# Performance work log

Measured on AMD Instinct MI355X. Metric: run time of the kernel, lower is better.

The kernel has to match this reference:

```python
import jax, jax.numpy as jnp
import numpy as np

B, T, V = 4, 2048, 2048
D, H, L = 512, 8, 4
HD = D // H


def setup_inputs() -> dict:
    key = jax.random.key(0)
    ks = jax.random.split(key, 8)
    inp = {
        "x": jax.random.normal(ks[0], (B, T, V), dtype=jnp.float32),
        "token_embedding": jax.random.normal(ks[1], (D, V), dtype=jnp.float32),
        "position_embedding": jax.random.normal(ks[2], (T, D), dtype=jnp.float32),
        "Wk": jax.random.normal(ks[3], (L, D, D), dtype=jnp.float32),
        "Wq": jax.random.normal(ks[4], (L, D, D), dtype=jnp.float32),
        "Wv": jax.random.normal(ks[5], (L, D, D), dtype=jnp.float32),
        "Wp": jax.random.normal(ks[6], (L, D, D), dtype=jnp.float32),
        "readout": jax.random.normal(ks[7], (V, D), dtype=jnp.float32),
    }
    return inp


def _attention_block(h, wk, wq, wv, wp):
    # h: [B, T, D]; weights [D, D] (inner_dim == D since head_dim*num_heads == D)
    b, t, c = h.shape
    s = c ** (-0.5)

    def proj(w):
        # F.linear(h, w) = h @ w.T -> [B,T,D] -> [B,H,T,HD], scaled by C^{-1/2}
        return (jnp.einsum('btc,dc->btd', h, w) * s).reshape(b, t, H, HD).transpose(0, 2, 1, 3)

    q, k, v = proj(wq), proj(wk), proj(wv)
    scores = jnp.einsum('bhqd,bhkd->bhqk', q, k) * (HD ** (-0.5))  # [B,H,T,T]
    attn = jax.nn.softmax(scores, axis=-1)
    out = jnp.einsum('bhqk,bhkd->bhqd', attn, v)  # [B,H,T,HD]
    out = out.transpose(0, 2, 1, 3).reshape(b, t, c)
    # projection.size(-1) == inner_dim == D
    return jnp.einsum('btc,oc->bto', out, wp) * (c ** (-0.5))


def reference(x, token_embedding, position_embedding, Wk, Wq, Wv, Wp, readout):
    b, t, c = x.shape  # c == vocab_size
    tok = jnp.einsum('btv,dv->btd', x, token_embedding) * (c ** (-0.5))
    h = tok + position_embedding[:t]
    for l in range(L):
        h = _attention_block(h, Wk[l], Wq[l], Wv[l], Wp[l])
    # logits on last token; readout.size(-1) == D
    logits = jnp.einsum('bd,vd->bv', h[:, -1, :], readout) * (D ** (-0.5))
    return logits
```

## Files before the change

kernel.cpp:

```cpp
#include <hip/hip_runtime.h>
#include <math.h>

typedef __attribute__((ext_vector_type(4)))  float    f32x4;
typedef __attribute__((ext_vector_type(16))) float    f32x16;
typedef __attribute__((ext_vector_type(2)))  _Float16 f16x2;
typedef __attribute__((ext_vector_type(4)))  _Float16 f16x4;
typedef __attribute__((ext_vector_type(8)))  _Float16 f16x8;
typedef __attribute__((ext_vector_type(4)))  unsigned u32x4;

constexpr int Bc  = 4;
constexpr int Tc  = 2048;
constexpr int Vc  = 2048;
constexpr int Dc  = 512;
constexpr int Hc  = 8;
constexpr int HDc = 64;
constexpr int Lc  = 4;
constexpr size_t SZe = (size_t)Bc * Tc * Dc;

constexpr float SM_C = 12.0f;

__device__ __forceinline__ void gload_lds16(const _Float16* g, _Float16* s) {
    __builtin_amdgcn_global_load_lds(
        (const __attribute__((address_space(1))) void*)g,
        (__attribute__((address_space(3))) void*)s,
        16, 0, 0);
}

__device__ __forceinline__ unsigned cvt_pk_u(float a, float b) {
    return __builtin_bit_cast(unsigned, __builtin_amdgcn_cvt_pkrtz(a, b));
}

__global__ __launch_bounds__(256) void cvt_k(
    const float* __restrict__ in, _Float16* __restrict__ out, int n4)
{
    for (int i = blockIdx.x * 256 + threadIdx.x; i < n4; i += gridDim.x * 256) {
        float4 v = ((const float4*)in)[i];
        f16x4 h = {(_Float16)v.x, (_Float16)v.y, (_Float16)v.z, (_Float16)v.w};
        *(f16x4*)&out[(size_t)i * 4] = h;
    }
}

__global__ __launch_bounds__(256) void cvtW_k(
    const float* __restrict__ a, const float* __restrict__ b,
    const float* __restrict__ c, const float* __restrict__ d,
    _Float16* __restrict__ oa, _Float16* __restrict__ ob,
    _Float16* __restrict__ oc, _Float16* __restrict__ od, int n4)
{
    const float* in; _Float16* out;
    switch (blockIdx.y) {
        case 0:  in = a; out = oa; break;
        case 1:  in = b; out = ob; break;
        case 2:  in = c; out = oc; break;
        default: in = d; out = od; break;
    }
    for (int i = blockIdx.x * 256 + threadIdx.x; i < n4; i += gridDim.x * 256) {
        float4 v = ((const float4*)in)[i];
        f16x4 h = {(_Float16)v.x, (_Float16)v.y, (_Float16)v.z, (_Float16)v.w};
        *(f16x4*)&out[(size_t)i * 4] = h;
    }
}


template<bool QKV>
__global__ __launch_bounds__(256) void gemm_f16(
    const _Float16* __restrict__ A,
    const _Float16* __restrict__ W0, const _Float16* __restrict__ W1,
    const _Float16* __restrict__ W2,
    void* __restrict__ C0, const float* __restrict__ pos,
    int K, float scA, float scB)
{
    __shared__ __align__(16) _Float16 LA[2][128 * 64];
    __shared__ __align__(16) _Float16 LB[2][64 * 64];

    const int tid = threadIdx.x;
    const int w  = tid >> 6, l = tid & 63;
    const int li = l & 15,  lg = l >> 4;
    const int wm = w >> 1,  wn = w & 1;
    const int m0 = blockIdx.x * 128;

    int sec = 0, n0;
    const _Float16* Wb;
    if (QKV) {
        sec = blockIdx.y >> 3; n0 = (blockIdx.y & 7) * 64;
        Wb = (sec == 0) ? W0 : ((sec == 1) ? W1 : W2);
    } else {
        n0 = blockIdx.y * 64; Wb = W0;
    }
    const float scale = (sec == 0) ? scA : scB;

    const _Float16* srcA[4];
    const _Float16* srcB[2];
#pragma unroll
    for (int i = 0; i < 4; ++i) {
        const int d = i * 4096 + tid * 16;
        const int r = d >> 7, cb = (d & 127) ^ ((r & 7) << 4);
        srcA[i] = A + (size_t)(m0 + r) * K + (cb >> 1);
    }
#pragma unroll
    for (int i = 0; i < 2; ++i) {
        const int d = i * 4096 + tid * 16;
        const int r = d >> 7, cb = (d & 127) ^ ((r & 7) << 4);
        srcB[i] = Wb + (size_t)(n0 + r) * K + (cb >> 1);
    }

    auto stage = [&](int b) {
#pragma unroll
        for (int i = 0; i < 4; ++i) { gload_lds16(srcA[i], &LA[b][i * 2048 + tid * 8]); srcA[i] += 64; }
#pragma unroll
        for (int i = 0; i < 2; ++i) { gload_lds16(srcB[i], &LB[b][i * 2048 + tid * 8]); srcB[i] += 64; }
    };

    f32x4 acc[4][2];
#pragma unroll
    for (int i = 0; i < 4; ++i)
#pragma unroll
        for (int j = 0; j < 2; ++j) acc[i][j] = (f32x4){0.f, 0.f, 0.f, 0.f};

    auto compute = [&](int b) {
        const char* Ab = (const char*)&LA[b][0];
        const char* Bb = (const char*)&LB[b][0];
        f16x8 af[4][2], bf[2][2];
#pragma unroll
        for (int mb = 0; mb < 4; ++mb) {
            const int row = wm * 64 + mb * 16 + li, sz = (row & 7) << 4;
#pragma unroll
            for (int fi = 0; fi < 2; ++fi)
                af[mb][fi] = *(const f16x8*)(Ab + row * 128 + ((fi * 64 + lg * 16) ^ sz));
        }
#pragma unroll
        for (int nb = 0; nb < 2; ++nb) {
            const int row = wn * 32 + nb * 16 + li, sz = (row & 7) << 4;
#pragma unroll
            for (int fi = 0; fi < 2; ++fi)
                bf[nb][fi] = *(const f16x8*)(Bb + row * 128 + ((fi * 64 + lg * 16) ^ sz));
        }
#pragma unroll
        for (int mb = 0; mb < 4; ++mb)
#pragma unroll
            for (int nb = 0; nb < 2; ++nb)
#pragma unroll
                for (int fi = 0; fi < 2; ++fi)
                    acc[mb][nb] = __builtin_amdgcn_mfma_f32_16x16x32_f16(
                        af[mb][fi], bf[nb][fi], acc[mb][nb], 0, 0, 0);
    };

    const int NTk = K >> 6;
    stage(0);
    for (int kt = 0; kt < NTk; ++kt) {
        const int cur = kt & 1;
        if (kt + 1 < NTk) {
            stage(cur ^ 1);
            asm volatile("s_waitcnt vmcnt(6)" ::: "memory");
        } else {
            asm volatile("s_waitcnt vmcnt(0)" ::: "memory");
        }
        __builtin_amdgcn_s_barrier();
        __builtin_amdgcn_sched_barrier(0);
        compute(cur);
        __builtin_amdgcn_s_barrier();
        __builtin_amdgcn_sched_barrier(0);
    }

#pragma unroll
    for (int mb = 0; mb < 4; ++mb) {
#pragma unroll
        for (int nb = 0; nb < 2; ++nb) {
            const int mbase = m0 + wm * 64 + mb * 16 + lg * 4;
            const int nc    = n0 + wn * 32 + nb * 16 + li;
            if (QKV && sec == 2) {
                const int t0 = mbase & (Tc - 1);
                const int bh2 = (mbase >> 11) * Hc + (nc >> 6), d = nc & 63;
                f16x4 vv;
#pragma unroll
                for (int r = 0; r < 4; ++r) vv[r] = (_Float16)(acc[mb][nb][r] * scale);
                _Float16* vf = (_Float16*)C0 + 2 * SZe;
                const size_t adr =
                    (((size_t)bh2 * 32 + (t0 >> 6)) * 8 + (d >> 5) * 4 + ((t0 >> 4) & 3)) * 512
                    + ((d & 31) + 32 * ((t0 >> 3) & 1)) * 8 + (t0 & 7);
                *(f16x4*)&vf[adr] = vv;
            } else if (QKV && sec == 1) {
                _Float16* kf = (_Float16*)C0 + SZe;
                const int t0 = mbase & (Tc - 1);
                const int bh2 = (mbase >> 11) * Hc + (nc >> 6), d = nc & 63;
                const size_t adr0 =
                    (((size_t)bh2 * 32 + (t0 >> 6)) * 8 + ((t0 >> 5) & 1) * 4 + (d >> 4)) * 512
                    + ((t0 & 31) + 32 * ((d >> 3) & 1)) * 8 + (d & 7);
#pragma unroll
                for (int r = 0; r < 4; ++r)
                    kf[adr0 + (size_t)r * 8] = (_Float16)(acc[mb][nb][r] * scale);
            } else if (QKV) {
                _Float16* outp = (_Float16*)C0;
#pragma unroll
                for (int r = 0; r < 4; ++r) {
                    const int m = mbase + r, bb2 = m >> 11, t = m & (Tc - 1);
                    outp[(((size_t)bb2 * Hc + (nc >> 6)) * Tc + t) * HDc + (nc & 63)] =
                        (_Float16)(acc[mb][nb][r] * scale);
                }
            } else {
                _Float16* outp = (_Float16*)C0;
#pragma unroll
                for (int r = 0; r < 4; ++r) {
                    const int m = mbase + r;
                    float val = acc[mb][nb][r] * scale;
                    if (pos) val += pos[(size_t)(m & (Tc - 1)) * Dc + nc];
                    outp[(size_t)m * Dc + nc] = (_Float16)val;
                }
            }
        }
    }
}

__global__ __launch_bounds__(256) void attn_mfma(
    const _Float16* __restrict__ Qh, const _Float16* __restrict__ Kf,
    const _Float16* __restrict__ Vf, _Float16* __restrict__ o)
{
    __shared__ __align__(16) _Float16 lds[16384];

    const int bid = blockIdx.x;
    const int bh  = bid & 31;
    const int qt  = bid >> 5;
    const int hh  = bh & (Hc - 1);
    const int bb  = bh >> 3;
    const int tid = threadIdx.x;
    const int w   = tid >> 6;
    const int l   = tid & 63;
    const int li  = l & 31, lg2 = l >> 5;
    const int qhalf = w & 1, khalf = w >> 1;
    const int q0  = qt * 64 + qhalf * 32;

    const _Float16* Qb = Qh + (size_t)bh * Tc * HDc;
    f16x8 qf[4];
#pragma unroll
    for (int fi = 0; fi < 4; ++fi)
        qf[fi] = *(const f16x8*)&Qb[(size_t)(q0 + li) * HDc + fi * 16 + lg2 * 8];

    const _Float16* sK = Kf + (size_t)bh * Tc * HDc + tid * 8;
    const _Float16* sV = Vf + (size_t)bh * Tc * HDc + tid * 8;
    auto stage = [&](int b) {
#pragma unroll
        for (int i = 0; i < 2; ++i) gload_lds16(sK + i * 2048, &lds[b * 4096 + i * 2048 + tid * 8]);
#pragma unroll
        for (int i = 0; i < 2; ++i) gload_lds16(sV + i * 2048, &lds[8192 + b * 4096 + i * 2048 + tid * 8]);
        sK += 4096; sV += 4096;
    };

    f32x16 oacc0, oacc1, sinit;
#pragma unroll
    for (int i = 0; i < 16; ++i) { oacc0[i] = 0.f; oacc1[i] = 0.f; sinit[i] = -SM_C; }
    float lrun = 0.f;

    stage(0);
    constexpr int NT = Tc / 64;
    for (int kt = 0; kt < NT; ++kt) {
        const int cur = kt & 1;
        if (kt + 1 < NT) {
            stage(cur ^ 1);
            asm volatile("s_waitcnt vmcnt(4)" ::: "memory");
        } else {
            asm volatile("s_waitcnt vmcnt(0)" ::: "memory");
        }
        __builtin_amdgcn_s_barrier();
        __builtin_amdgcn_sched_barrier(0);

        const _Float16* KL = &lds[cur * 4096];
        const _Float16* VL = &lds[8192 + cur * 4096];

        __builtin_amdgcn_s_setprio(1);
        f16x8 k0 = *(const f16x8*)(KL + (khalf * 4 + 0) * 512 + l * 8);
        f32x16 s = __builtin_amdgcn_mfma_f32_32x32x16_f16(k0, qf[0], sinit, 0, 0, 0);
#pragma unroll
        for (int fi = 1; fi < 4; ++fi) {
            f16x8 ka = *(const f16x8*)(KL + (khalf * 4 + fi) * 512 + l * 8);
            s = __builtin_amdgcn_mfma_f32_32x32x16_f16(ka, qf[fi], s, 0, 0, 0);
        }
        __builtin_amdgcn_s_setprio(0);

        unsigned cc[8];
        float ls0 = 0.f, ls1 = 0.f;
#pragma unroll
        for (int g = 0; g < 4; ++g) {
            float p0 = __builtin_amdgcn_exp2f(s[4 * g + 0]);
            float p1 = __builtin_amdgcn_exp2f(s[4 * g + 1]);
            float p2 = __builtin_amdgcn_exp2f(s[4 * g + 2]);
            float p3 = __builtin_amdgcn_exp2f(s[4 * g + 3]);
            ls0 += p0 + p1; ls1 += p2 + p3;
            cc[2 * g]     = cvt_pk_u(p0, p1);
            cc[2 * g + 1] = cvt_pk_u(p2, p3);
        }
        lrun += ls0 + ls1;

        f16x8 Bf[2];
#pragma unroll
        for (int m = 0; m < 2; ++m) {
            auto u = __builtin_amdgcn_permlane32_swap(cc[m * 4 + 0], cc[m * 4 + 2], false, false);
            auto v = __builtin_amdgcn_permlane32_swap(cc[m * 4 + 1], cc[m * 4 + 3], false, false);
            u32x4 b4 = (u32x4){u[0], v[0], u[1], v[1]};
            Bf[m] = __builtin_bit_cast(f16x8, b4);
        }

        __builtin_amdgcn_s_setprio(1);
#pragma unroll
        for (int m = 0; m < 2; ++m) {
            f16x8 v0 = *(const f16x8*)(VL + (0 + khalf * 2 + m) * 512 + l * 8);
            f16x8 v1 = *(const f16x8*)(VL + (4 + khalf * 2 + m) * 512 + l * 8);
            oacc0 = __builtin_amdgcn_mfma_f32_32x32x16_f16(v0, Bf[m], oacc0, 0, 0, 0);
            oacc1 = __builtin_amdgcn_mfma_f32_32x32x16_f16(v1, Bf[m], oacc1, 0, 0, 0);
        }
        __builtin_amdgcn_s_setprio(0);

        __builtin_amdgcn_s_barrier();
        __builtin_amdgcn_sched_barrier(0);
    }

    lrun += __shfl_xor(lrun, 32);
    float* cm = (float*)lds;
    const int cbase = qhalf * (64 * 33) + l * 33;
    if (khalf == 1) {
#pragma unroll
        for (int i = 0; i < 16; ++i) cm[cbase + i]      = oacc0[i];
#pragma unroll
        for (int i = 0; i < 16; ++i) cm[cbase + 16 + i] = oacc1[i];
        cm[cbase + 32] = lrun;
    }
    __syncthreads();
    if (khalf == 0) {
#pragma unroll
        for (int i = 0; i < 16; ++i) oacc0[i] += cm[cbase + i];
#pragma unroll
        for (int i = 0; i < 16; ++i) oacc1[i] += cm[cbase + 16 + i];
        lrun += cm[cbase + 32];

        const float inv = 1.f / lrun;
        _Float16* op = o + ((size_t)(bb * Tc + q0 + li) * Dc + hh * HDc);
#pragma unroll
        for (int g = 0; g < 4; ++g) {
            const int d0 = 8 * g + 4 * lg2;
            f16x4 r0 = {(_Float16)(oacc0[4 * g + 0] * inv), (_Float16)(oacc0[4 * g + 1] * inv),
                        (_Float16)(oacc0[4 * g + 2] * inv), (_Float16)(oacc0[4 * g + 3] * inv)};
            f16x4 r1 = {(_Float16)(oacc1[4 * g + 0] * inv), (_Float16)(oacc1[4 * g + 1] * inv),
                        (_Float16)(oacc1[4 * g + 2] * inv), (_Float16)(oacc1[4 * g + 3] * inv)};
            *(f16x4*)(op + d0)      = r0;
            *(f16x4*)(op + 32 + d0) = r1;
        }
    }
}

__global__ __launch_bounds__(256) void readout_k(
    const _Float16* __restrict__ h, const float* __restrict__ ro,
    float* __restrict__ out, float scale)
{
    const int idx = blockIdx.x * 256 + threadIdx.x;
    const int vv  = idx & (Vc - 1);
    const int bb  = idx >> 11;
    const _Float16* hp = h + (size_t)(bb * Tc + (Tc - 1)) * Dc;
    const float* rp = ro + (size_t)vv * Dc;
    float ax = 0.f, ay = 0.f, az = 0.f, aw = 0.f;
#pragma unroll 8
    for (int i = 0; i < Dc / 4; ++i) {
        f16x4  hv = *(const f16x4*)(hp + i * 4);
        float4 rv = *(const float4*)(rp + i * 4);
        ax = fmaf((float)hv[0], rv.x, ax);
        ay = fmaf((float)hv[1], rv.y, ay);
        az = fmaf((float)hv[2], rv.z, az);
        aw = fmaf((float)hv[3], rv.w, aw);
    }
    out[idx] = ((ax + ay) + (az + aw)) * scale;
}

extern "C" void kernel_launch(void* const* d_in, const int* in_sizes, int n_in,
                              void* d_out, int out_size, void* d_ws, size_t ws_size,
                              hipStream_t stream)
{
    const float* x    = (const float*)d_in[0];
    const float* temb = (const float*)d_in[1];
    const float* pemb = (const float*)d_in[2];
    const float* Wk   = (const float*)d_in[3];
    const float* Wq   = (const float*)d_in[4];
    const float* Wv   = (const float*)d_in[5];
    const float* Wp   = (const float*)d_in[6];
    const float* ro   = (const float*)d_in[7];
    float* out = (float*)d_out;

    _Float16* h16    = (_Float16*)d_ws;
    _Float16* temb16 = h16 + SZe;
    _Float16* wq16   = temb16 + (size_t)Dc * Vc;
    _Float16* wk16   = wq16 + (size_t)Lc * Dc * Dc;
    _Float16* wv16   = wk16 + (size_t)Lc * Dc * Dc;
    _Float16* wp16   = wv16 + (size_t)Lc * Dc * Dc;
    _Float16* o16    = wp16 + (size_t)Lc * Dc * Dc;
    _Float16* qh     = o16 + SZe;
    _Float16* khF    = qh + SZe;
    _Float16* vhF    = khF + SZe;
    _Float16* x16    = o16;

    const float s_emb  = 1.0f / sqrtf((float)Vc);
    const float s_proj = 1.0f / sqrtf((float)Dc);
    const float s_q    = s_proj * 0.125f * 1.44269504f;

    const int W4 = Lc * Dc * Dc / 4;
    cvt_k<<<2048, 256, 0, stream>>>(x, x16, (int)SZe);
    cvt_k<<<512, 256, 0, stream>>>(temb, temb16, Dc * Vc / 4);
    cvtW_k<<<dim3(512, 4), 256, 0, stream>>>(Wq, Wk, Wv, Wp,
                                             wq16, wk16, wv16, wp16, W4);

    gemm_f16<false><<<dim3(64, 8), 256, 0, stream>>>(
        x16, temb16, nullptr, nullptr, h16, pemb, Vc, s_emb, s_emb);

    const size_t WOFF = (size_t)Dc * Dc;
    for (int lyr = 0; lyr < Lc; ++lyr) {
        gemm_f16<true><<<dim3(64, 24), 256, 0, stream>>>(
            h16, wq16 + lyr * WOFF, wk16 + lyr * WOFF, wv16 + lyr * WOFF,
            qh, nullptr, Dc, s_q, s_proj);

        attn_mfma<<<Bc * Hc * (Tc / 64), 256, 0, stream>>>(qh, khF, vhF, o16);

        gemm_f16<false><<<dim3(64, 8), 256, 0, stream>>>(
            o16, wp16 + lyr * WOFF, nullptr, nullptr, h16, nullptr, Dc, s_proj, s_proj);
    }

    readout_k<<<(Bc * Vc) / 256, 256, 0, stream>>>(h16, ro, out, s_proj);
}
```

Before: 407.7 us.

## Load K/V fragments directly from global into registers in attention kernel

Replaces the double-buffered global-to-LDS staging of K and V tiles in the attention kernel with per-wave direct global loads into register fragments, prefetched one iteration ahead. This removes LDS traffic and the per-iteration block barriers. The cost is that each K/V element is now fetched from global/L2 by both query-half waves instead of once per block, and load latency is hidden only by a single iteration of software prefetch. LDS is shrunk to just the final cross-wave reduction buffer, which could raise occupancy.

Result: no change. 401.1 us (-1.6%).

```diff
diff --git a/kernel.cpp b/kernel.cpp
--- a/kernel.cpp
+++ b/kernel.cpp
@@ -214,7 +214,7 @@
     const _Float16* __restrict__ Qh, const _Float16* __restrict__ Kf,
     const _Float16* __restrict__ Vf, _Float16* __restrict__ o)
 {
-    __shared__ __align__(16) _Float16 lds[16384];
+    __shared__ float cm[4224];
 
     const int bid = blockIdx.x;
     const int bh  = bid & 31;
@@ -234,46 +234,40 @@
     for (int fi = 0; fi < 4; ++fi)
         qf[fi] = *(const f16x8*)&Qb[(size_t)(q0 + li) * HDc + fi * 16 + lg2 * 8];
 
-    const _Float16* sK = Kf + (size_t)bh * Tc * HDc + tid * 8;
-    const _Float16* sV = Vf + (size_t)bh * Tc * HDc + tid * 8;
-    auto stage = [&](int b) {
-#pragma unroll
-        for (int i = 0; i < 2; ++i) gload_lds16(sK + i * 2048, &lds[b * 4096 + i * 2048 + tid * 8]);
-#pragma unroll
-        for (int i = 0; i < 2; ++i) gload_lds16(sV + i * 2048, &lds[8192 + b * 4096 + i * 2048 + tid * 8]);
-        sK += 4096; sV += 4096;
-    };
+    const _Float16* Kb  = Kf + (size_t)bh * Tc * HDc + (khalf * 4) * 512 + l * 8;
+    const _Float16* Vb0 = Vf + (size_t)bh * Tc * HDc + (khalf * 2) * 512 + l * 8;
+    const _Float16* Vb1 = Vb0 + 4 * 512;
 
     f32x16 oacc0, oacc1, sinit;
 #pragma unroll
     for (int i = 0; i < 16; ++i) { oacc0[i] = 0.f; oacc1[i] = 0.f; sinit[i] = -SM_C; }
     float lrun = 0.f;
 
-    stage(0);
+    f16x8 kfr[4], vfr[4];
+#pragma unroll
+    for (int fi = 0; fi < 4; ++fi) kfr[fi] = *(const f16x8*)(Kb + fi * 512);
+#pragma unroll
+    for (int m = 0; m < 2; ++m) {
+        vfr[m]     = *(const f16x8*)(Vb0 + m * 512);
+        vfr[2 + m] = *(const f16x8*)(Vb1 + m * 512);
+    }
+    Kb += 4096; Vb0 += 4096; Vb1 += 4096;
+
     constexpr int NT = Tc / 64;
     for (int kt = 0; kt < NT; ++kt) {
-        const int cur = kt & 1;
+        __builtin_amdgcn_s_setprio(1);
+        f32x16 s = __builtin_amdgcn_mfma_f32_32x32x16_f16(kfr[0], qf[0], sinit, 0, 0, 0);
+        s = __builtin_amdgcn_mfma_f32_32x32x16_f16(kfr[1], qf[1], s, 0, 0, 0);
+        s = __builtin_amdgcn_mfma_f32_32x32x16_f16(kfr[2], qf[2], s, 0, 0, 0);
+        s = __builtin_amdgcn_mfma_f32_32x32x16_f16(kfr[3], qf[3], s, 0, 0, 0);
+        __builtin_amdgcn_s_setprio(0);
+
         if (kt + 1 < NT) {
-            stage(cur ^ 1);
-            asm volatile("s_waitcnt vmcnt(4)" ::: "memory");
-        } else {
-            asm volatile("s_waitcnt vmcnt(0)" ::: "memory");
-        }
-        __builtin_amdgcn_s_barrier();
+#pragma unroll
+            for (int fi = 0; fi < 4; ++fi) kfr[fi] = *(const f16x8*)(Kb + fi * 512);
+            Kb += 4096;
+        }
         __builtin_amdgcn_sched_barrier(0);
-
-        const _Float16* KL = &lds[cur * 4096];
-        const _Float16* VL = &lds[8192 + cur * 4096];
-
-        __builtin_amdgcn_s_setprio(1);
-        f16x8 k0 = *(const f16x8*)(KL + (khalf * 4 + 0) * 512 + l * 8);
-        f32x16 s = __builtin_amdgcn_mfma_f32_32x32x16_f16(k0, qf[0], sinit, 0, 0, 0);
-#pragma unroll
-        for (int fi = 1; fi < 4; ++fi) {
-            f16x8 ka = *(const f16x8*)(KL + (khalf * 4 + fi) * 512 + l * 8);
-            s = __builtin_amdgcn_mfma_f32_32x32x16_f16(ka, qf[fi], s, 0, 0, 0);
-        }
-        __builtin_amdgcn_s_setprio(0);
 
         unsigned cc[8];
         float ls0 = 0.f, ls1 = 0.f;
@@ -299,21 +293,24 @@
         }
 
         __builtin_amdgcn_s_setprio(1);
-#pragma unroll
-        for (int m = 0; m < 2; ++m) {
-            f16x8 v0 = *(const f16x8*)(VL + (0 + khalf * 2 + m) * 512 + l * 8);
-            f16x8 v1 = *(const f16x8*)(VL + (4 + khalf * 2 + m) * 512 + l * 8);
-            oacc0 = __builtin_amdgcn_mfma_f32_32x32x16_f16(v0, Bf[m], oacc0, 0, 0, 0);
-            oacc1 = __builtin_amdgcn_mfma_f32_32x32x16_f16(v1, Bf[m], oacc1, 0, 0, 0);
-        }
+        oacc0 = __builtin_amdgcn_mfma_f32_32x32x16_f16(vfr[0], Bf[0], oacc0, 0, 0, 0);
+        oacc0 = __builtin_amdgcn_mfma_f32_32x32x16_f16(vfr[1], Bf[1], oacc0, 0, 0, 0);
+        oacc1 = __builtin_amdgcn_mfma_f32_32x32x16_f16(vfr[2], Bf[0], oacc1, 0, 0, 0);
+        oacc1 = __builtin_amdgcn_mfma_f32_32x32x16_f16(vfr[3], Bf[1], oacc1, 0, 0, 0);
         __builtin_amdgcn_s_setprio(0);
 
-        __builtin_amdgcn_s_barrier();
+        if (kt + 1 < NT) {
+#pragma unroll
+            for (int m = 0; m < 2; ++m) {
+                vfr[m]     = *(const f16x8*)(Vb0 + m * 512);
+                vfr[2 + m] = *(const f16x8*)(Vb1 + m * 512);
+            }
+            Vb0 += 4096; Vb1 += 4096;
+        }
         __builtin_amdgcn_sched_barrier(0);
     }
 
     lrun += __shfl_xor(lrun, 32);
-    float* cm = (float*)lds;
     const int cbase = qhalf * (64 * 33) + l * 33;
     if (khalf == 1) {
 #pragma unroll
```
